# Kernel tuning notes

Measured on AMD Instinct MI355X. Metric: run time of the kernel, lower is better.

The kernel has to match this reference:

```python
import jax, jax.numpy as jnp
import numpy as np

B, H, HKV, QLEN, KVLEN, D = 4, 32, 8, 16, 8192, 128


def setup_inputs() -> dict:
    key = jax.random.key(0)
    ks = jax.random.split(key, 7)
    query = jax.random.normal(ks[0], (B, H, QLEN, D), dtype=jnp.float32)
    # INT8 KV caches (stored as int8, dequantized in the hot path)
    key_cache = jax.random.randint(ks[1], (B, HKV, KVLEN, D), -127, 128).astype(jnp.int8)
    value_cache = jax.random.randint(ks[2], (B, HKV, KVLEN, D), -127, 128).astype(jnp.int8)
    # per-(batch, kv_head, token) quant params, broadcast over head_dim
    key_scale = jax.random.uniform(ks[3], (B, HKV, KVLEN), dtype=jnp.float32, minval=0.005, maxval=0.02)
    key_zero = jax.random.normal(ks[4], (B, HKV, KVLEN), dtype=jnp.float32)
    value_scale = jax.random.uniform(ks[5], (B, HKV, KVLEN), dtype=jnp.float32, minval=0.005, maxval=0.02)
    value_zero = jax.random.normal(ks[6], (B, HKV, KVLEN), dtype=jnp.float32)
    return {
        "query": query,
        "key_cache": key_cache,
        "value_cache": value_cache,
        "key_scale": key_scale,
        "key_zero": key_zero,
        "value_scale": value_scale,
        "value_zero": value_zero,
    }


def _dequant(x_q, scale, zero, dtype):
    # (x_q - zero) * scale, params broadcast over head_dim
    return ((x_q.astype(jnp.float32) - zero[..., None]) * scale[..., None]).astype(dtype)


def reference(query, key_cache, value_cache, key_scale, key_zero, value_scale, value_zero):
    b, h, qlen, d = query.shape
    hkv = key_cache.shape[1]
    n_rep = h // hkv  # GQA: each kv head serves n_rep query heads
    scale = jnp.asarray(d, query.dtype) ** -0.5

    k = _dequant(key_cache, key_scale, key_zero, query.dtype)   # [b, hkv, kv, d]
    v = _dequant(value_cache, value_scale, value_zero, query.dtype)

    # Grouped einsum == repeat_interleave of K/V along heads, without materializing copies
    qg = query.reshape(b, hkv, n_rep, qlen, d)
    scores = jnp.einsum('bgrqd,bgkd->bgrqk', qg, k) * scale      # [b, hkv, n_rep, q, kv]
    attn = jax.nn.softmax(scores, axis=-1)
    out = jnp.einsum('bgrqk,bgkd->bgrqd', attn, v)
    return out.reshape(b, h, qlen, d)
```

## Files before the change

kernel.cpp:

```cpp
#include <hip/hip_runtime.h>
#include <hip/hip_bf16.h>
#include <stdint.h>

#define Bc    4
#define Hc    32
#define HKVc  8
#define QLc   16
#define KVc   8192
#define Dc    128
#define NREPc 4
#define THR   8.0f

typedef _Float16 f16x8 __attribute__((ext_vector_type(8)));
typedef _Float16 f16x4 __attribute__((ext_vector_type(4)));
typedef float f32x4  __attribute__((ext_vector_type(4)));
typedef int   i32x4  __attribute__((ext_vector_type(4)));
typedef uint32_t u32x2 __attribute__((ext_vector_type(2)));

__device__ __forceinline__ uint32_t pk1152(int x0, int x1) {
  return (__builtin_amdgcn_perm((uint32_t)x1, (uint32_t)x0, 0x05040100u)
          & 0x00FF00FFu) ^ 0x64806480u;
}

#define BAR() do {                                            \
    asm volatile("s_waitcnt lgkmcnt(0)" ::: "memory");        \
    __builtin_amdgcn_sched_barrier(0);                        \
    __builtin_amdgcn_s_barrier();                             \
  } while (0)

__global__ __launch_bounds__(256) void attn_partial(
    const float* __restrict__ q, const int* __restrict__ kc,
    const int* __restrict__ vc,
    const float* __restrict__ ksc, const float* __restrict__ kzr,
    const float* __restrict__ vsc, const float* __restrict__ vzr,
    float* __restrict__ ws_acc, float* __restrict__ ws_m,
    float* __restrict__ ws_l, int nsplit)
{
  __shared__ __align__(16) unsigned short Klds[32][128];
  __shared__ __align__(16) unsigned short Vlds[128][40];
  __shared__ __align__(16) float          Sl[4][256];

  const int bid   = blockIdx.x;
  const int split = bid % nsplit;
  const int bg    = bid / nsplit;
  const int chunk = KVc / nsplit;
  const int t_begin = split * chunk;
  const int nt    = chunk >> 5;

  const int tid  = threadIdx.x;
  const int wave = tid >> 6;
  const int lane = tid & 63;
  const int l15  = lane & 15;
  const int lg   = lane >> 4;

  const int b = bg >> 3, g = bg & 7;
  const int h = (g << 2) + wave;

  f16x8 qa[4];
  float qsum = 0.f;
  const float* qrow = q + ((size_t)((b * Hc + h) * QLc + l15)) * Dc;
#pragma unroll
  for (int ks = 0; ks < 4; ++ks) {
    const f32x4* qv = (const f32x4*)(qrow + ks * 32 + (lg << 3));
    f32x4 qlo = qv[0], qhi = qv[1];
    f16x8 f;
#pragma unroll
    for (int j = 0; j < 4; ++j) {
      f[j]     = (_Float16)qlo[j];
      f[4 + j] = (_Float16)qhi[j];
      qsum += (float)f[j] + (float)f[4 + j];
    }
    qa[ks] = f;
  }
  qsum += __shfl_xor(qsum, 16);
  qsum += __shfl_xor(qsum, 32);

  const float QK_SCALE = 0.088388347648f * 1.44269504089f;

  float m = -1e30f, ell = 0.f, corr = 0.f;
  f32x4 acc[8];
#pragma unroll
  for (int dt = 0; dt < 8; ++dt) acc[dt] = (f32x4){0.f, 0.f, 0.f, 0.f};

  const int*   kb   = kc  + (size_t)bg * KVc * Dc;
  const int*   vb   = vc  + (size_t)bg * KVc * Dc;
  const float* kscb = ksc + (size_t)bg * KVc;
  const float* kzrb = kzr + (size_t)bg * KVc;
  const float* vscb = vsc + (size_t)bg * KVc;
  const float* vzrb = vzr + (size_t)bg * KVc;

  const int kt  = tid >> 3;
  const int kd  = (tid & 7) << 4;
  const int ksw = (kt & 7) << 3;
  const int tq  = tid >> 5;
  const int dq  = (tid & 31) << 2;
  const int tb  = (tq << 2) ^ ((((dq >> 4) & 3)) << 3);

  i32x4 kpA[4], vpA[4], kpB[4], vpB[4];

#define ISSUE(KP, VP, TILE) do {                                             \
    const int _t0 = t_begin + ((TILE) << 5);                                 \
    const int* _ks = kb + (size_t)(_t0 + kt) * Dc + kd;                      \
    KP[0] = ((const i32x4*)_ks)[0]; KP[1] = ((const i32x4*)_ks)[1];          \
    KP[2] = ((const i32x4*)_ks)[2]; KP[3] = ((const i32x4*)_ks)[3];          \
    VP[0] = *(const i32x4*)(vb + (size_t)(_t0 + (tq << 2) + 0) * Dc + dq);   \
    VP[1] = *(const i32x4*)(vb + (size_t)(_t0 + (tq << 2) + 1) * Dc + dq);   \
    VP[2] = *(const i32x4*)(vb + (size_t)(_t0 + (tq << 2) + 2) * Dc + dq);   \
    VP[3] = *(const i32x4*)(vb + (size_t)(_t0 + (tq << 2) + 3) * Dc + dq);   \
  } while (0)

#define WRITE(KP, VP) do {                                                   \
    i32x4 _kA, _kB;                                                          \
    _kA[0]=(int)pk1152(KP[0][0],KP[0][1]); _kA[1]=(int)pk1152(KP[0][2],KP[0][3]); \
    _kA[2]=(int)pk1152(KP[1][0],KP[1][1]); _kA[3]=(int)pk1152(KP[1][2],KP[1][3]); \
    _kB[0]=(int)pk1152(KP[2][0],KP[2][1]); _kB[1]=(int)pk1152(KP[2][2],KP[2][3]); \
    _kB[2]=(int)pk1152(KP[3][0],KP[3][1]); _kB[3]=(int)pk1152(KP[3][2],KP[3][3]); \
    *(i32x4*)&Klds[kt][kd ^ ksw]       = _kA;                                \
    *(i32x4*)&Klds[kt][(kd + 8) ^ ksw] = _kB;                                \
    _Pragma("unroll")                                                        \
    for (int _j = 0; _j < 4; ++_j) {                                         \
      u32x2 _pk;                                                             \
      _pk[0] = pk1152(VP[0][_j], VP[1][_j]);                                 \
      _pk[1] = pk1152(VP[2][_j], VP[3][_j]);                                 \
      *(u32x2*)&Vlds[dq + _j][tb] = _pk;                                     \
    }                                                                        \
  } while (0)

#define RESTAGE(WBASE) do {                                                  \
    const int _arr = tid >> 6;                                               \
    const int _sl  = (tid & 63) << 2;                                        \
    int _toff = _sl;                                                         \
    if (_toff > chunk - 4) _toff = chunk - 4;                                \
    const float* _sp = (_arr == 0) ? kscb : (_arr == 1) ? kzrb               \
                     : (_arr == 2) ? vscb : vzrb;                            \
    f32x4 _sv = *(const f32x4*)(_sp + (WBASE) + _toff);                      \
    if (_arr == 0) { _sv[0]*=QK_SCALE; _sv[1]*=QK_SCALE;                     \
                     _sv[2]*=QK_SCALE; _sv[3]*=QK_SCALE; }                   \
    else if (_arr == 2) { _sv[0]*=1024.f; _sv[1]*=1024.f;                    \
                          _sv[2]*=1024.f; _sv[3]*=1024.f; }                  \
    else { _sv[0]+=1152.f; _sv[1]+=1152.f; _sv[2]+=1152.f; _sv[3]+=1152.f; } \
    *(f32x4*)&Sl[_arr][_sl] = _sv;                                           \
  } while (0)

  ISSUE(kpA, vpA, 0);
  RESTAGE(t_begin);
  WRITE(kpA, vpA);
  if (nt > 1) ISSUE(kpA, vpA, 1);
  if (nt > 2) ISSUE(kpB, vpB, 2);
  BAR();

  for (int it = 0; it < nt; ++it) {
    if (it && !(it & 7)) {
      RESTAGE(t_begin + ((it >> 3) << 8));
      BAR();
    }

    const int tw = (it & 7) << 5;
    const f32x4 ksc0 = *(const f32x4*)&Sl[0][tw + (lg << 2)];
    const f32x4 ksc1 = *(const f32x4*)&Sl[0][tw + 16 + (lg << 2)];
    const f32x4 kzr0 = *(const f32x4*)&Sl[1][tw + (lg << 2)];
    const f32x4 kzr1 = *(const f32x4*)&Sl[1][tw + 16 + (lg << 2)];
    const f32x4 vsc0 = *(const f32x4*)&Sl[2][tw + (lg << 2)];
    const f32x4 vsc1 = *(const f32x4*)&Sl[2][tw + 16 + (lg << 2)];
    const f32x4 vzr0 = *(const f32x4*)&Sl[3][tw + (lg << 2)];
    const f32x4 vzr1 = *(const f32x4*)&Sl[3][tw + 16 + (lg << 2)];

    f32x4 sA0 = (f32x4){0.f,0.f,0.f,0.f}, sA1 = (f32x4){0.f,0.f,0.f,0.f};
    f32x4 sB0 = (f32x4){0.f,0.f,0.f,0.f}, sB1 = (f32x4){0.f,0.f,0.f,0.f};
    __builtin_amdgcn_s_setprio(1);
#pragma unroll
    for (int ks = 0; ks < 2; ++ks) {
      f16x8 kfA = *(const f16x8*)
          &Klds[l15][(ks * 32 + (lg << 3)) ^ ((l15 & 7) << 3)];
      sA0 = __builtin_amdgcn_mfma_f32_16x16x32_f16(kfA, qa[ks], sA0, 0, 0, 0);
      f16x8 kfB = *(const f16x8*)
          &Klds[16 + l15][(ks * 32 + (lg << 3)) ^ ((l15 & 7) << 3)];
      sB0 = __builtin_amdgcn_mfma_f32_16x16x32_f16(kfB, qa[ks], sB0, 0, 0, 0);
    }
#pragma unroll
    for (int ks = 2; ks < 4; ++ks) {
      f16x8 kfA = *(const f16x8*)
          &Klds[l15][(ks * 32 + (lg << 3)) ^ ((l15 & 7) << 3)];
      sA1 = __builtin_amdgcn_mfma_f32_16x16x32_f16(kfA, qa[ks], sA1, 0, 0, 0);
      f16x8 kfB = *(const f16x8*)
          &Klds[16 + l15][(ks * 32 + (lg << 3)) ^ ((l15 & 7) << 3)];
      sB1 = __builtin_amdgcn_mfma_f32_16x16x32_f16(kfB, qa[ks], sB1, 0, 0, 0);
    }
    __builtin_amdgcn_s_setprio(0);
    const f32x4 scA = sA0 + sA1;
    const f32x4 scB = sB0 + sB1;

    float s0[4], s1[4];
#pragma unroll
    for (int j = 0; j < 4; ++j) {
      s0[j] = ksc0[j] * (scA[j] - kzr0[j] * qsum);
      s1[j] = ksc1[j] * (scB[j] - kzr1[j] * qsum);
    }

    float tm = fmaxf(fmaxf(fmaxf(s0[0], s0[1]), fmaxf(s0[2], s0[3])),
                     fmaxf(fmaxf(s1[0], s1[1]), fmaxf(s1[2], s1[3])));
    tm = fmaxf(tm, __shfl_xor(tm, 16));
    tm = fmaxf(tm, __shfl_xor(tm, 32));
    if (__any(tm > m + THR)) {
      float nm = fmaxf(m, tm);
      float cf = exp2f(m - nm);
      m = nm;
      ell *= cf; corr *= cf;
      float cfq[4];
#pragma unroll
      for (int j = 0; j < 4; ++j) cfq[j] = __shfl(cf, (lg << 2) + j);
#pragma unroll
      for (int dt = 0; dt < 8; ++dt)
#pragma unroll
        for (int j = 0; j < 4; ++j) acc[dt][j] *= cfq[j];
    }

    f16x8 pp;
#pragma unroll
    for (int j = 0; j < 4; ++j) {
      float pA = exp2f(s0[j] - m);
      float pB = exp2f(s1[j] - m);
      ell += pA + pB;
      _Float16 ca = (_Float16)(pA * vsc0[j]);
      _Float16 cb = (_Float16)(pB * vsc1[j]);
      corr += (float)ca * vzr0[j] + (float)cb * vzr1[j];
      pp[j]     = ca;
      pp[4 + j] = cb;
    }

    __builtin_amdgcn_s_setprio(1);
#pragma unroll
    for (int dt = 0; dt < 8; ++dt) {
      const int swz = (dt & 3) << 3;
      f16x4 vA = *(const f16x4*)&Vlds[(dt << 4) + l15][(lg << 2) ^ swz];
      f16x4 vB = *(const f16x4*)&Vlds[(dt << 4) + l15][(16 + (lg << 2)) ^ swz];
      f16x8 vf = __builtin_shufflevector(vA, vB, 0, 1, 2, 3, 4, 5, 6, 7);
      acc[dt] = __builtin_amdgcn_mfma_f32_16x16x32_f16(pp, vf, acc[dt], 0, 0, 0);
    }
    __builtin_amdgcn_s_setprio(0);

    if (it + 1 < nt) {
      if (it & 1) {
        BAR();
        WRITE(kpB, vpB);
        if (it + 3 < nt) ISSUE(kpB, vpB, it + 3);
        BAR();
      } else {
        BAR();
        WRITE(kpA, vpA);
        if (it + 3 < nt) ISSUE(kpA, vpA, it + 3);
        BAR();
      }
    }
  }

  ell += __shfl_xor(ell, 16);  ell += __shfl_xor(ell, 32);
  corr += __shfl_xor(corr, 16); corr += __shfl_xor(corr, 32);
  float corrq[4];
#pragma unroll
  for (int j = 0; j < 4; ++j) corrq[j] = __shfl(corr, (lg << 2) + j);

  const size_t pbase = ((size_t)bg * nsplit + split) * 64;
  const float inv1k = 0.0009765625f;
#pragma unroll
  for (int dt = 0; dt < 8; ++dt)
#pragma unroll
    for (int j = 0; j < 4; ++j) {
      int row = (wave << 4) + (lg << 2) + j;
      int d   = (dt << 4) + l15;
      ws_acc[(pbase + row) * Dc + d] = (acc[dt][j] - corrq[j]) * inv1k;
    }
  if (lg == 0) {
    ws_m[pbase + (wave << 4) + l15] = m;
    ws_l[pbase + (wave << 4) + l15] = ell;
  }
#undef ISSUE
#undef WRITE
#undef RESTAGE
}

__global__ __launch_bounds__(128) void attn_combine(
    const float* __restrict__ ws_acc, const float* __restrict__ ws_m,
    const float* __restrict__ ws_l, float* __restrict__ out, int nsplit)
{
  const int r   = blockIdx.x;
  const int bg  = r >> 6;
  const int row = r & 63;
  const int d   = threadIdx.x;

  float M = -1e30f;
#pragma unroll 4
  for (int i = 0; i < nsplit; ++i)
    M = fmaxf(M, ws_m[((size_t)bg * nsplit + i) * 64 + row]);
  float L = 0.f, o = 0.f;
#pragma unroll 4
  for (int i = 0; i < nsplit; ++i) {
    size_t pb = ((size_t)bg * nsplit + i) * 64 + row;
    float w = exp2f(ws_m[pb] - M);
    L += ws_l[pb] * w;
    o += ws_acc[pb * Dc + d] * w;
  }
  const int b = bg >> 3, g = bg & 7;
  const int rep = row >> 4, qq = row & 15;
  out[(((size_t)(b * Hc + g * NREPc + rep)) * QLc + qq) * Dc + d] = o / L;
}

extern "C" void kernel_launch(void* const* d_in, const int* in_sizes, int n_in,
                              void* d_out, int out_size, void* d_ws,
                              size_t ws_size, hipStream_t stream) {
  const float* q   = (const float*)d_in[0];
  const int*   kc  = (const int*)d_in[1];
  const int*   vc  = (const int*)d_in[2];
  const float* ksc = (const float*)d_in[3];
  const float* kzr = (const float*)d_in[4];
  const float* vsc = (const float*)d_in[5];
  const float* vzr = (const float*)d_in[6];
  float* out = (float*)d_out;

  int nsplit = 32;
  while (nsplit > 1) {
    size_t need = (size_t)32 * nsplit * 64 * (Dc + 2) * sizeof(float);
    if (need <= ws_size) break;
    nsplit >>= 1;
  }
  float* ws_acc = (float*)d_ws;
  float* ws_m   = ws_acc + (size_t)32 * nsplit * 64 * Dc;
  float* ws_l   = ws_m   + (size_t)32 * nsplit * 64;

  attn_partial<<<dim3(32 * nsplit), dim3(256), 0, stream>>>(
      q, kc, vc, ksc, kzr, vsc, vzr, ws_acc, ws_m, ws_l, nsplit);
  attn_combine<<<dim3(32 * 64), dim3(128), 0, stream>>>(
      ws_acc, ws_m, ws_l, out, nsplit);
}
```

Baseline: 79.11 us.

## Double-buffer K/V tiles in LDS and drop to one barrier per iteration

K and V shared-memory tiles are now double-buffered. The next tile is written into the alternate buffer at the start of each iteration, before the QK and PV MFMAs run on the current buffer. This cuts the two barriers per iteration, one before and one after the LDS write, down to one at the end. The aim is to overlap LDS staging with compute and reduce synchronisation stalls. The cost is roughly double the K/V LDS footprint, and the V row padding shrinks from 40 to 36, which may change bank-conflict behaviour and occupancy.

```diff
diff --git a/kernel.cpp b/kernel.cpp
--- a/kernel.cpp
+++ b/kernel.cpp
@@ -36,8 +36,8 @@
     float* __restrict__ ws_acc, float* __restrict__ ws_m,
     float* __restrict__ ws_l, int nsplit)
 {
-  __shared__ __align__(16) unsigned short Klds[32][128];
-  __shared__ __align__(16) unsigned short Vlds[128][40];
+  __shared__ __align__(16) unsigned short Klds[2][32][128];
+  __shared__ __align__(16) unsigned short Vlds[2][128][36];
   __shared__ __align__(16) float          Sl[4][256];
 
   const int bid   = blockIdx.x;
@@ -109,20 +109,20 @@
     VP[3] = *(const i32x4*)(vb + (size_t)(_t0 + (tq << 2) + 3) * Dc + dq);   \
   } while (0)
 
-#define WRITE(KP, VP) do {                                                   \
+#define WRITE(KP, VP, BUF) do {                                              \
     i32x4 _kA, _kB;                                                          \
     _kA[0]=(int)pk1152(KP[0][0],KP[0][1]); _kA[1]=(int)pk1152(KP[0][2],KP[0][3]); \
     _kA[2]=(int)pk1152(KP[1][0],KP[1][1]); _kA[3]=(int)pk1152(KP[1][2],KP[1][3]); \
     _kB[0]=(int)pk1152(KP[2][0],KP[2][1]); _kB[1]=(int)pk1152(KP[2][2],KP[2][3]); \
     _kB[2]=(int)pk1152(KP[3][0],KP[3][1]); _kB[3]=(int)pk1152(KP[3][2],KP[3][3]); \
-    *(i32x4*)&Klds[kt][kd ^ ksw]       = _kA;                                \
-    *(i32x4*)&Klds[kt][(kd + 8) ^ ksw] = _kB;                                \
+    *(i32x4*)&Klds[BUF][kt][kd ^ ksw]       = _kA;                           \
+    *(i32x4*)&Klds[BUF][kt][(kd + 8) ^ ksw] = _kB;                           \
     _Pragma("unroll")                                                        \
     for (int _j = 0; _j < 4; ++_j) {                                         \
       u32x2 _pk;                                                             \
       _pk[0] = pk1152(VP[0][_j], VP[1][_j]);                                 \
       _pk[1] = pk1152(VP[2][_j], VP[3][_j]);                                 \
-      *(u32x2*)&Vlds[dq + _j][tb] = _pk;                                     \
+      *(u32x2*)&Vlds[BUF][dq + _j][tb] = _pk;                                \
     }                                                                        \
   } while (0)
 
@@ -144,15 +144,27 @@
 
   ISSUE(kpA, vpA, 0);
   RESTAGE(t_begin);
-  WRITE(kpA, vpA);
+  WRITE(kpA, vpA, 0);
   if (nt > 1) ISSUE(kpA, vpA, 1);
   if (nt > 2) ISSUE(kpB, vpB, 2);
   BAR();
 
   for (int it = 0; it < nt; ++it) {
+    const int cur = it & 1;
+
     if (it && !(it & 7)) {
       RESTAGE(t_begin + ((it >> 3) << 8));
       BAR();
+    }
+
+    if (it + 1 < nt) {
+      if ((it + 1) & 1) {
+        WRITE(kpA, vpA, cur ^ 1);
+        if (it + 3 < nt) ISSUE(kpA, vpA, it + 3);
+      } else {
+        WRITE(kpB, vpB, cur ^ 1);
+        if (it + 3 < nt) ISSUE(kpB, vpB, it + 3);
+      }
     }
 
     const int tw = (it & 7) << 5;
@@ -171,19 +183,19 @@
 #pragma unroll
     for (int ks = 0; ks < 2; ++ks) {
       f16x8 kfA = *(const f16x8*)
-          &Klds[l15][(ks * 32 + (lg << 3)) ^ ((l15 & 7) << 3)];
+          &Klds[cur][l15][(ks * 32 + (lg << 3)) ^ ((l15 & 7) << 3)];
       sA0 = __builtin_amdgcn_mfma_f32_16x16x32_f16(kfA, qa[ks], sA0, 0, 0, 0);
       f16x8 kfB = *(const f16x8*)
-          &Klds[16 + l15][(ks * 32 + (lg << 3)) ^ ((l15 & 7) << 3)];
+          &Klds[cur][16 + l15][(ks * 32 + (lg << 3)) ^ ((l15 & 7) << 3)];
       sB0 = __builtin_amdgcn_mfma_f32_16x16x32_f16(kfB, qa[ks], sB0, 0, 0, 0);
     }
 #pragma unroll
     for (int ks = 2; ks < 4; ++ks) {
       f16x8 kfA = *(const f16x8*)
-          &Klds[l15][(ks * 32 + (lg << 3)) ^ ((l15 & 7) << 3)];
+          &Klds[cur][l15][(ks * 32 + (lg << 3)) ^ ((l15 & 7) << 3)];
       sA1 = __builtin_amdgcn_mfma_f32_16x16x32_f16(kfA, qa[ks], sA1, 0, 0, 0);
       f16x8 kfB = *(const f16x8*)
-          &Klds[16 + l15][(ks * 32 + (lg << 3)) ^ ((l15 & 7) << 3)];
+          &Klds[cur][16 + l15][(ks * 32 + (lg << 3)) ^ ((l15 & 7) << 3)];
       sB1 = __builtin_amdgcn_mfma_f32_16x16x32_f16(kfB, qa[ks], sB1, 0, 0, 0);
     }
     __builtin_amdgcn_s_setprio(0);
@@ -232,26 +244,14 @@
 #pragma unroll
     for (int dt = 0; dt < 8; ++dt) {
       const int swz = (dt & 3) << 3;
-      f16x4 vA = *(const f16x4*)&Vlds[(dt << 4) + l15][(lg << 2) ^ swz];
-      f16x4 vB = *(const f16x4*)&Vlds[(dt << 4) + l15][(16 + (lg << 2)) ^ swz];
+      f16x4 vA = *(const f16x4*)&Vlds[cur][(dt << 4) + l15][(lg << 2) ^ swz];
+      f16x4 vB = *(const f16x4*)&Vlds[cur][(dt << 4) + l15][(16 + (lg << 2)) ^ swz];
       f16x8 vf = __builtin_shufflevector(vA, vB, 0, 1, 2, 3, 4, 5, 6, 7);
       acc[dt] = __builtin_amdgcn_mfma_f32_16x16x32_f16(pp, vf, acc[dt], 0, 0, 0);
     }
     __builtin_amdgcn_s_setprio(0);
 
-    if (it + 1 < nt) {
-      if (it & 1) {
-        BAR();
-        WRITE(kpB, vpB);
-        if (it + 3 < nt) ISSUE(kpB, vpB, it + 3);
-        BAR();
-      } else {
-        BAR();
-        WRITE(kpA, vpA);
-        if (it + 3 < nt) ISSUE(kpA, vpA, it + 3);
-        BAR();
-      }
-    }
+    if (it + 1 < nt) BAR();
   }
 
   ell += __shfl_xor(ell, 16);  ell += __shfl_xor(ell, 32);
```

New measurement: 80.88 us. 1.02x slower.
